# Kernel tuning notes

Hardware: AMD Instinct MI355X
Metric: run time of the kernel (lower is better)

## Reference

```python
import jax, jax.numpy as jnp
import numpy as np

B, S, D = 2, 2048, 2048
H, G = 16, 4
DH = D // H  # 128
KV = G * DH  # 512


def setup_inputs() -> dict:
    key = jax.random.key(0)
    ks = jax.random.split(key, 10)
    scale = 1.0 / np.sqrt(D)
    hidden_state = jax.random.normal(ks[0], (B, S, D), dtype=jnp.float32)
    # causal mask: 1 above the diagonal (positions to block), 0 elsewhere
    casual_mask = jnp.triu(jnp.ones((S, S), dtype=jnp.float32), k=1)
    padding_mask = jnp.zeros((B, S), dtype=jnp.float32)
    Wq = jax.random.normal(ks[1], (D, D), dtype=jnp.float32) * scale
    bq = jnp.zeros((D,), dtype=jnp.float32)
    Wk = jax.random.normal(ks[2], (D, KV), dtype=jnp.float32) * scale
    bk = jnp.zeros((KV,), dtype=jnp.float32)
    Wv = jax.random.normal(ks[3], (D, KV), dtype=jnp.float32) * scale
    bv = jnp.zeros((KV,), dtype=jnp.float32)
    Wo = jax.random.normal(ks[4], (D, D), dtype=jnp.float32) * scale
    bo = jnp.zeros((D,), dtype=jnp.float32)
    return {"hidden_state": hidden_state, "casual_mask": casual_mask,
            "padding_mask": padding_mask, "Wq": Wq, "bq": bq, "Wk": Wk,
            "bk": bk, "Wv": Wv, "bv": bv, "Wo": Wo, "bo": bo}


def reference(hidden_state, casual_mask, padding_mask, Wq, bq, Wk, bk, Wv, bv, Wo, bo):
    b, s, _ = hidden_state.shape
    rep = H // G  # heads per KV group
    q = (hidden_state @ Wq + bq).reshape(b, s, H, DH).transpose(0, 2, 1, 3)  # [b,H,s,dh]
    k = (hidden_state @ Wk + bk).reshape(b, s, G, DH).transpose(0, 2, 1, 3)  # [b,G,s,dh]
    v = (hidden_state @ Wv + bv).reshape(b, s, G, DH).transpose(0, 2, 1, 3)
    # expand KV heads: each group serves H//G query heads
    k = jnp.repeat(k, rep, axis=1)  # [b,H,s,dh]
    v = jnp.repeat(v, rep, axis=1)
    scores = jnp.einsum('bhqd,bhkd->bhqk', q, k) / jnp.sqrt(jnp.float32(DH))
    scores = scores + casual_mask * (-1e9)
    scores = scores + padding_mask[:, None, None, :] * (-1e9)
    attn = jax.nn.softmax(scores, axis=-1)
    out = jnp.einsum('bhqk,bhkd->bhqd', attn, v)  # [b,H,s,dh]
    out = out.transpose(0, 2, 1, 3).reshape(b, s, D)
    return out @ Wo + bo
```

## Files before the change

### kernel.cpp

```cpp
#include <hip/hip_runtime.h>
#include <math.h>

typedef unsigned short u16;
typedef __bf16 bf16_t;
typedef u16 u16x4 __attribute__((ext_vector_type(4)));
typedef u16 u16x8 __attribute__((ext_vector_type(8)));
typedef bf16_t bf16x8 __attribute__((ext_vector_type(8)));
typedef float f32x4 __attribute__((ext_vector_type(4)));

__device__ __forceinline__ float bf2f(u16 v) {
    union { unsigned u; float f; } x; x.u = ((unsigned)v) << 16; return x.f;
}
__device__ __forceinline__ u16 f2bf(float f) {
    union { float f; unsigned u; } x; x.f = f;
    unsigned u = x.u;
    return (u16)((u + 0x7fffu + ((u >> 16) & 1u)) >> 16);
}

__device__ __forceinline__ void gload16(const u16* g, u16* l) {
    __builtin_amdgcn_global_load_lds(
        (const __attribute__((address_space(1))) void*)g,
        (__attribute__((address_space(3))) void*)l,
        16, 0, 0);
}

#define POWS_UNITS 436

__device__ __forceinline__ bool is_bf16_input(const unsigned* __restrict__ probe) {
    unsigned w = probe[(threadIdx.x & 63) * 32771 + 7];
    unsigned b7 = (w >> 8) & 0x7f;
    bool hit = (b7 >= 0x38) && (b7 <= 0x3f);
    return __builtin_popcountll(__ballot(hit)) >= 32;
}

__global__ __launch_bounds__(256) void prep_kernel(
    const void* __restrict__ X, u16* __restrict__ Xc,
    const void* __restrict__ Wq, const void* __restrict__ Wk,
    const void* __restrict__ Wv, u16* __restrict__ WqkvT,
    const unsigned* __restrict__ probe)
{
    __shared__ u16 t[32][33];
    const bool bf = is_bf16_input(probe);
    const int bid = blockIdx.x;

    if (bid < 4096) {
        int i = (bid * 256 + threadIdx.x) * 8;
        if (bf) {
            *(u16x8*)&Xc[i] = *(const u16x8*)&((const u16*)X)[i];
        } else {
            const float* s = (const float*)X + i;
            u16x8 o;
#pragma unroll
            for (int j = 0; j < 8; j++) o[j] = f2bf(s[j]);
            *(u16x8*)&Xc[i] = o;
        }
        return;
    }

    const void* in; u16* out; int R, C, bx, by;
    if (bid < 8192) {
        int b2 = bid - 4096; in = Wq; out = WqkvT;
        R = 2048; C = 2048; bx = (b2 & 63) * 32; by = (b2 >> 6) * 32;
    } else if (bid < 9216) {
        int b2 = bid - 8192; in = Wk; out = WqkvT + 2048 * 2048;
        R = 2048; C = 512; bx = (b2 & 15) * 32; by = (b2 >> 4) * 32;
    } else {
        int b2 = bid - 9216; in = Wv; out = WqkvT + 2560 * 2048;
        R = 2048; C = 512; bx = (b2 & 15) * 32; by = (b2 >> 4) * 32;
    }
    int x = threadIdx.x & 31, y = threadIdx.x >> 5;
    if (bf) {
        const u16* s = (const u16*)in;
#pragma unroll
        for (int i = 0; i < 32; i += 8)
            t[y + i][x] = s[(size_t)(by + y + i) * C + bx + x];
    } else {
        const float* s = (const float*)in;
#pragma unroll
        for (int i = 0; i < 32; i += 8)
            t[y + i][x] = f2bf(s[(size_t)(by + y + i) * C + bx + x]);
    }
    __syncthreads();
#pragma unroll
    for (int i = 0; i < 32; i += 8)
        out[(size_t)(bx + y + i) * R + by + x] = t[x][y + i];
}

__global__ __launch_bounds__(256) void tconv_kernel(
    const void* __restrict__ in, u16* __restrict__ out, int R, int C,
    const unsigned* __restrict__ probe)
{
    bool bf = is_bf16_input(probe);
    __shared__ u16 t[32][33];
    int x = threadIdx.x & 31, y = threadIdx.x >> 5;
    int bx = blockIdx.x * 32, by = blockIdx.y * 32;
    if (bf) {
        const u16* s = (const u16*)in;
#pragma unroll
        for (int i = 0; i < 32; i += 8)
            t[y + i][x] = s[(size_t)(by + y + i) * C + bx + x];
    } else {
        const float* s = (const float*)in;
#pragma unroll
        for (int i = 0; i < 32; i += 8)
            t[y + i][x] = f2bf(s[(size_t)(by + y + i) * C + bx + x]);
    }
    __syncthreads();
#pragma unroll
    for (int i = 0; i < 32; i += 8)
        out[(size_t)(bx + y + i) * R + by + x] = t[x][y + i];
}

__global__ __launch_bounds__(256) void transpose_kernel(
    const u16* __restrict__ in, u16* __restrict__ out, int R, int LD)
{
    __shared__ u16 t[32][33];
    int x = threadIdx.x & 31, y = threadIdx.x >> 5;
    int bx = blockIdx.x * 32, by = blockIdx.y * 32;
#pragma unroll
    for (int i = 0; i < 32; i += 8)
        t[y + i][x] = in[(size_t)(by + y + i) * LD + bx + x];
    __syncthreads();
#pragma unroll
    for (int i = 0; i < 32; i += 8)
        out[(size_t)(bx + y + i) * R + by + x] = t[x][y + i];
}

__global__ __launch_bounds__(256) void gemm_bias_kernel(
    const u16* __restrict__ A, const u16* __restrict__ BT,
    const void* __restrict__ bias0, const void* __restrict__ bias1,
    const void* __restrict__ bias2, void* __restrict__ Cout,
    int M, int N, int K, const unsigned* __restrict__ probe,
    int out_native, float scale)
{
    __shared__ __align__(16) u16 As[128 * 32];
    __shared__ __align__(16) u16 Bs[128 * 32];
    const int tid  = threadIdx.x;
    const int lane = tid & 63, wave = tid >> 6;
    const int quad = lane >> 4, li = lane & 15;
    const int bm = blockIdx.x * 128, bn = blockIdx.y * 128;
    const int wm = (wave >> 1) * 64, wn = (wave & 1) * 64;
    const int lrow = lane >> 2;
    const int lcol = (lane & 3) * 8;

    f32x4 acc[4][4] = {};

    for (int k0 = 0; k0 < K; k0 += 32) {
#pragma unroll
        for (int j = 0; j < 2; j++) {
            int c = wave * 2 + j;
            int row = c * 16 + lrow;
            gload16(&A [(size_t)(bm + row) * K + k0 + lcol], &As[c * 16 * 32]);
            gload16(&BT[(size_t)(bn + row) * K + k0 + lcol], &Bs[c * 16 * 32]);
        }
        __syncthreads();
        bf16x8 af[4], bfr[4];
#pragma unroll
        for (int i = 0; i < 4; i++)
            af[i]  = *(const bf16x8*)&As[(wm + i * 16 + li) * 32 + quad * 8];
#pragma unroll
        for (int i = 0; i < 4; i++)
            bfr[i] = *(const bf16x8*)&Bs[(wn + i * 16 + li) * 32 + quad * 8];
#pragma unroll
        for (int mt = 0; mt < 4; mt++)
#pragma unroll
            for (int nt = 0; nt < 4; nt++)
                acc[mt][nt] = __builtin_amdgcn_mfma_f32_16x16x32_bf16(
                    af[mt], bfr[nt], acc[mt][nt], 0, 0, 0);
        __syncthreads();
    }

    const bool bf_in = is_bf16_input(probe);
    const bool out_bf = out_native ? bf_in : true;
#pragma unroll
    for (int nt = 0; nt < 4; nt++) {
        int col = bn + wn + nt * 16 + li;
        const void* bp; int bc;
        if (col < 2048)      { bp = bias0; bc = col; }
        else if (col < 2560) { bp = bias1; bc = col - 2048; }
        else                 { bp = bias2; bc = col - 2560; }
        float bb = bf_in ? bf2f(((const u16*)bp)[bc]) : ((const float*)bp)[bc];
        if (out_bf) {
            u16* C16 = (u16*)Cout;
#pragma unroll
            for (int mt = 0; mt < 4; mt++)
#pragma unroll
                for (int r = 0; r < 4; r++) {
                    int row = bm + wm + mt * 16 + quad * 4 + r;
                    C16[(size_t)row * N + col] = f2bf((acc[mt][nt][r] + bb) * scale);
                }
        } else {
            float* Cf = (float*)Cout;
#pragma unroll
            for (int mt = 0; mt < 4; mt++)
#pragma unroll
                for (int r = 0; r < 4; r++) {
                    int row = bm + wm + mt * 16 + quad * 4 + r;
                    Cf[(size_t)row * N + col] = (acc[mt][nt][r] + bb) * scale;
                }
        }
    }
}

__global__ __launch_bounds__(256) void flash_kernel(
    const u16* __restrict__ Q, const u16* __restrict__ Kg,
    const u16* __restrict__ VT, u16* __restrict__ O,
    float* __restrict__ POws, float* __restrict__ POdout,
    float* __restrict__ PM, float* __restrict__ PL)
{
    constexpr int S = 2048, D = 2048, DH = 128, QKSTR = 3072;
    constexpr float SCALE = 0.08838834764831845f;
    __shared__ __align__(16) u16 Ks[32 * 136];
    __shared__ __align__(16) u16 Vt[128 * 40];
    __shared__ __align__(16) u16 Pw[4][32 * 40];

    const int tid  = threadIdx.x;
    const int wave = tid >> 6, lane = tid & 63;
    const int quad = lane >> 4, li = lane & 15;
    const int uu = blockIdx.x, h = blockIdx.y, b = blockIdx.z;
    int qt, cc, nc;
    if (uu < 7)       { qt = uu;                         cc = 0;          nc = 1; }
    else if (uu < 21) { int t = uu - 7;  qt = 7 + (t >> 1);  cc = t & 1;  nc = 2; }
    else              { int t = uu - 21; qt = 14 + t / 3;    cc = t % 3;  nc = 3; }
    const int T = qt + 1;
    const int tb = T / nc, trem = T % nc;
    const int tcnt = tb + (cc < trem ? 1 : 0);
    const int tstart = cc * tb + (cc < trem ? cc : trem);
    const int kstart = tstart * 128;
    const int kend   = (tstart + tcnt) * 128;
    const int g = h >> 2;
    const int q0w = qt * 128 + wave * 32;

    const u16* Qb = Q  + (size_t)b * S * QKSTR;
    const u16* Kb = Kg + (size_t)b * S * QKSTR;
    const u16* Vg = VT + (size_t)g * DH * (2 * S) + (size_t)b * S;

    bf16x8 qf[2][4];
#pragma unroll
    for (int m = 0; m < 2; m++)
#pragma unroll
        for (int c = 0; c < 4; c++)
            qf[m][c] = *(const bf16x8*)&Qb[(size_t)(q0w + m * 16 + li) * QKSTR
                                           + h * DH + c * 32 + quad * 8];

    f32x4 oacc[2][8] = {};
    float mr[2] = { -INFINITY, -INFINITY };
    float lr[2] = { 0.f, 0.f };

    u16x8 kreg[2], vreg[2];
#pragma unroll
    for (int ch = 0; ch < 2; ch++) {
        int idx = tid + ch * 256;
        kreg[ch] = *(const u16x8*)&Kb[(size_t)(kstart + (idx >> 4)) * QKSTR
                                      + g * DH + (idx & 15) * 8];
        vreg[ch] = *(const u16x8*)&Vg[(size_t)(idx >> 2) * (2 * S)
                                      + kstart + (idx & 3) * 8];
    }

    for (int kc = kstart; kc < kend; kc += 32) {
#pragma unroll
        for (int ch = 0; ch < 2; ch++) {
            int idx = tid + ch * 256;
            *(u16x8*)&Ks[(idx >> 4) * 136 + (idx & 15) * 8] = kreg[ch];
            *(u16x8*)&Vt[(idx >> 2) * 40  + (idx & 3) * 8]  = vreg[ch];
        }
        __syncthreads();

        int kn = kc + 32;
        if (kn < kend) {
#pragma unroll
            for (int ch = 0; ch < 2; ch++) {
                int idx = tid + ch * 256;
                kreg[ch] = *(const u16x8*)&Kb[(size_t)(kn + (idx >> 4)) * QKSTR
                                              + g * DH + (idx & 15) * 8];
                vreg[ch] = *(const u16x8*)&Vg[(size_t)(idx >> 2) * (2 * S)
                                              + kn + (idx & 3) * 8];
            }
        }

        if (kc <= q0w) {
            f32x4 sacc[2][2] = {};
#pragma unroll
            for (int t = 0; t < 2; t++)
#pragma unroll
                for (int c = 0; c < 4; c++) {
                    bf16x8 kf = *(const bf16x8*)&Ks[(t * 16 + li) * 136 + c * 32 + quad * 8];
#pragma unroll
                    for (int m = 0; m < 2; m++)
                        sacc[m][t] = __builtin_amdgcn_mfma_f32_16x16x32_bf16(
                            kf, qf[m][c], sacc[m][t], 0, 0, 0);
                }

            float alpha_b[2][4];
#pragma unroll
            for (int m = 0; m < 2; m++) {
                int row = q0w + m * 16 + li;
                f32x4 s0 = sacc[m][0] * SCALE;
                f32x4 s1 = sacc[m][1] * SCALE;
#pragma unroll
                for (int r = 0; r < 4; r++) {
                    int k0 = kc + quad * 4 + r;
                    if (k0 > row)      s0[r] = -INFINITY;
                    if (k0 + 16 > row) s1[r] = -INFINITY;
                }
                float mx = fmaxf(fmaxf(fmaxf(s0[0], s0[1]), fmaxf(s0[2], s0[3])),
                                 fmaxf(fmaxf(s1[0], s1[1]), fmaxf(s1[2], s1[3])));
                mx = fmaxf(mx, __shfl_xor(mx, 16));
                mx = fmaxf(mx, __shfl_xor(mx, 32));
                float mnew = fmaxf(mr[m], mx);
                float al = __expf(mr[m] - mnew);
                mr[m] = mnew;
                f32x4 p0, p1;
                float ps = 0.f;
#pragma unroll
                for (int r = 0; r < 4; r++) {
                    p0[r] = __expf(s0[r] - mnew);
                    p1[r] = __expf(s1[r] - mnew);
                    ps += p0[r] + p1[r];
                }
                ps += __shfl_xor(ps, 16);
                ps += __shfl_xor(ps, 32);
                lr[m] = lr[m] * al + ps;
                u16x4 c0, c1;
#pragma unroll
                for (int r = 0; r < 4; r++) { c0[r] = f2bf(p0[r]); c1[r] = f2bf(p1[r]); }
                *(u16x4*)&Pw[wave][(m * 16 + li) * 40 + quad * 4]      = c0;
                *(u16x4*)&Pw[wave][(m * 16 + li) * 40 + 16 + quad * 4] = c1;
#pragma unroll
                for (int r = 0; r < 4; r++)
                    alpha_b[m][r] = __shfl(al, quad * 4 + r, 16);
            }

#pragma unroll
            for (int m = 0; m < 2; m++)
#pragma unroll
                for (int dt = 0; dt < 8; dt++)
#pragma unroll
                    for (int r = 0; r < 4; r++)
                        oacc[m][dt][r] *= alpha_b[m][r];

            asm volatile("s_waitcnt lgkmcnt(0)" ::: "memory");
            union { u16x8 u; bf16x8 bv; } pc0, pc1;
            pc0.u = *(const u16x8*)&Pw[wave][(0 * 16 + li) * 40 + quad * 8];
            pc1.u = *(const u16x8*)&Pw[wave][(1 * 16 + li) * 40 + quad * 8];
            bf16x8 pf[2] = { pc0.bv, pc1.bv };

#pragma unroll
            for (int dt = 0; dt < 8; dt++) {
                bf16x8 vf = *(const bf16x8*)&Vt[(dt * 16 + li) * 40 + quad * 8];
#pragma unroll
                for (int m = 0; m < 2; m++)
                    oacc[m][dt] = __builtin_amdgcn_mfma_f32_16x16x32_bf16(
                        pf[m], vf, oacc[m][dt], 0, 0, 0);
            }
        }
        __syncthreads();
    }

    if (nc == 1) {
        u16* Ob = O + (size_t)b * S * D;
#pragma unroll
        for (int m = 0; m < 2; m++) {
#pragma unroll
            for (int r = 0; r < 4; r++) {
                float linv = 1.0f / __shfl(lr[m], quad * 4 + r, 16);
                int row = q0w + m * 16 + quad * 4 + r;
#pragma unroll
                for (int dt = 0; dt < 8; dt++)
                    Ob[(size_t)row * D + h * DH + dt * 16 + li] =
                        f2bf(oacc[m][dt][r] * linv);
            }
        }
    } else {
        const int pl = (qt <= 13) ? (qt - 7) * 2 + cc : 14 + (qt - 14) * 3 + cc;
        const int pg = (b * 16 + h) * 20 + pl;
        float* POu = (pg < POWS_UNITS)
                   ? (POws   + (size_t)pg * 16384)
                   : (POdout + (size_t)(pg - POWS_UNITS) * 16384);
#pragma unroll
        for (int m = 0; m < 2; m++)
#pragma unroll
            for (int r = 0; r < 4; r++) {
                int rl = wave * 32 + m * 16 + quad * 4 + r;
#pragma unroll
                for (int dt = 0; dt < 8; dt++)
                    POu[rl * 128 + dt * 16 + li] = oacc[m][dt][r];
            }
        if (quad == 0) {
#pragma unroll
            for (int m = 0; m < 2; m++) {
                int rl = wave * 32 + m * 16 + li;
                PM[pg * 128 + rl] = mr[m];
                PL[pg * 128 + rl] = lr[m];
            }
        }
    }
}

__global__ __launch_bounds__(256) void combine_kernel(
    const float* __restrict__ POws, const float* __restrict__ POdout,
    const float* __restrict__ PM, const float* __restrict__ PL,
    u16* __restrict__ O)
{
    constexpr int S = 2048, D = 2048;
    const int qt = 7 + blockIdx.x, h = blockIdx.y, b = blockIdx.z;
    const int nc = (qt <= 13) ? 2 : 3;
    const int pl0 = (qt <= 13) ? (qt - 7) * 2 : 14 + (qt - 14) * 3;
    const int pg0 = (b * 16 + h) * 20 + pl0;
    const int t = threadIdx.x;
    const int row = t >> 1, half = (t & 1) * 64;

    float m[3], l[3], w[3];
    const float* p[3];
    float M = -INFINITY;
    for (int i = 0; i < nc; i++) {
        int pg = pg0 + i;
        m[i] = PM[pg * 128 + row];
        l[i] = PL[pg * 128 + row];
        M = fmaxf(M, m[i]);
        p[i] = ((pg < POWS_UNITS)
                ? (POws   + (size_t)pg * 16384)
                : (POdout + (size_t)(pg - POWS_UNITS) * 16384))
               + row * 128 + half;
    }
    float lsum = 0.f;
    for (int i = 0; i < nc; i++) { w[i] = __expf(m[i] - M); lsum += w[i] * l[i]; }
    float linv = 1.0f / lsum;

    u16* out = O + (size_t)(b * S + qt * 128 + row) * D + h * 128 + half;
#pragma unroll 4
    for (int j = 0; j < 64; j += 4) {
        f32x4 acc = {};
        for (int i = 0; i < nc; i++) {
            f32x4 a = *(const f32x4*)&p[i][j];
#pragma unroll
            for (int e = 0; e < 4; e++) acc[e] += a[e] * w[i];
        }
        u16x4 o;
#pragma unroll
        for (int e = 0; e < 4; e++) o[e] = f2bf(acc[e] * linv);
        *(u16x4*)&out[j] = o;
    }
}

extern "C" void kernel_launch(void* const* d_in, const int* in_sizes, int n_in,
                              void* d_out, int out_size, void* d_ws, size_t ws_size,
                              hipStream_t stream)
{
    const void* X  = d_in[0];
    const void* Wq = d_in[3];
    const void* bq = d_in[4];
    const void* Wk = d_in[5];
    const void* bk = d_in[6];
    const void* Wv = d_in[7];
    const void* bv = d_in[8];
    const void* Wo = d_in[9];
    const void* bo = d_in[10];
    const unsigned* probe = (const unsigned*)d_in[3];

    u16* ws    = (u16*)d_ws;
    u16* Xc    = ws;
    u16* WqkvT = Xc    + 8388608;
    u16* QKV   = WqkvT + 6291456;
    u16* VTb   = QKV   + 12582912;
    u16* Ob    = VTb   + 2097152;
    float* POws   = (float*)ws;
    float* PM     = POws + (size_t)POWS_UNITS * 16384;
    float* PL     = PM + 640 * 128;
    float* POdout = (float*)d_out;

    prep_kernel<<<10240, 256, 0, stream>>>(X, Xc, Wq, Wk, Wv, WqkvT, probe);

    gemm_bias_kernel<<<dim3(32, 24), 256, 0, stream>>>(
        Xc, WqkvT, bq, bk, bv, QKV, 4096, 3072, 2048, probe, 0, 1.0f);

    transpose_kernel<<<dim3(16, 128), 256, 0, stream>>>(QKV + 2560, VTb, 4096, 3072);

    flash_kernel<<<dim3(27, 16, 2), 256, 0, stream>>>(
        QKV, QKV + 2048, VTb, Ob, POws, POdout, PM, PL);

    combine_kernel<<<dim3(9, 16, 2), 256, 0, stream>>>(POws, POdout, PM, PL, Ob);

    tconv_kernel<<<dim3(64, 64), 256, 0, stream>>>(Wo, WqkvT, 2048, 2048, probe);

    gemm_bias_kernel<<<dim3(32, 16), 256, 0, stream>>>(
        Ob, WqkvT, bo, bo, bo, d_out, 4096, 2048, 2048, probe, 1, 1.0f);
}
```

Baseline: 416.6 us.

## Fuse V transpose into QKV GEMM epilogue and merge combine with Wo transpose

The QKV GEMM epilogue now also writes the V columns transposed into the VT buffer, so the separate transpose kernel is gone. The split-K combine and the Wo transpose/convert are merged into one launch, with the block index selecting the role. The transposed Wo is written into the QKV region, which is no longer needed at that point. This removes two kernel launches and one extra read of V, at the cost of strided scalar stores in the GEMM epilogue for V tiles.

```diff
diff --git a/kernel.cpp b/kernel.cpp
--- a/kernel.cpp
+++ b/kernel.cpp
@@ -86,52 +86,12 @@
         out[(size_t)(bx + y + i) * R + by + x] = t[x][y + i];
 }
 
-__global__ __launch_bounds__(256) void tconv_kernel(
-    const void* __restrict__ in, u16* __restrict__ out, int R, int C,
-    const unsigned* __restrict__ probe)
-{
-    bool bf = is_bf16_input(probe);
-    __shared__ u16 t[32][33];
-    int x = threadIdx.x & 31, y = threadIdx.x >> 5;
-    int bx = blockIdx.x * 32, by = blockIdx.y * 32;
-    if (bf) {
-        const u16* s = (const u16*)in;
-#pragma unroll
-        for (int i = 0; i < 32; i += 8)
-            t[y + i][x] = s[(size_t)(by + y + i) * C + bx + x];
-    } else {
-        const float* s = (const float*)in;
-#pragma unroll
-        for (int i = 0; i < 32; i += 8)
-            t[y + i][x] = f2bf(s[(size_t)(by + y + i) * C + bx + x]);
-    }
-    __syncthreads();
-#pragma unroll
-    for (int i = 0; i < 32; i += 8)
-        out[(size_t)(bx + y + i) * R + by + x] = t[x][y + i];
-}
-
-__global__ __launch_bounds__(256) void transpose_kernel(
-    const u16* __restrict__ in, u16* __restrict__ out, int R, int LD)
-{
-    __shared__ u16 t[32][33];
-    int x = threadIdx.x & 31, y = threadIdx.x >> 5;
-    int bx = blockIdx.x * 32, by = blockIdx.y * 32;
-#pragma unroll
-    for (int i = 0; i < 32; i += 8)
-        t[y + i][x] = in[(size_t)(by + y + i) * LD + bx + x];
-    __syncthreads();
-#pragma unroll
-    for (int i = 0; i < 32; i += 8)
-        out[(size_t)(bx + y + i) * R + by + x] = t[x][y + i];
-}
-
 __global__ __launch_bounds__(256) void gemm_bias_kernel(
     const u16* __restrict__ A, const u16* __restrict__ BT,
     const void* __restrict__ bias0, const void* __restrict__ bias1,
     const void* __restrict__ bias2, void* __restrict__ Cout,
     int M, int N, int K, const unsigned* __restrict__ probe,
-    int out_native, float scale)
+    int out_native, float scale, u16* __restrict__ VTdual)
 {
     __shared__ __align__(16) u16 As[128 * 32];
     __shared__ __align__(16) u16 Bs[128 * 32];
@@ -182,12 +142,16 @@
         float bb = bf_in ? bf2f(((const u16*)bp)[bc]) : ((const float*)bp)[bc];
         if (out_bf) {
             u16* C16 = (u16*)Cout;
+            const bool dv = (VTdual != nullptr) && (col >= 2560);
+            u16* vtp = dv ? &VTdual[(size_t)(col - 2560) * 4096] : nullptr;
 #pragma unroll
             for (int mt = 0; mt < 4; mt++)
 #pragma unroll
                 for (int r = 0; r < 4; r++) {
                     int row = bm + wm + mt * 16 + quad * 4 + r;
-                    C16[(size_t)row * N + col] = f2bf((acc[mt][nt][r] + bb) * scale);
+                    u16 v = f2bf((acc[mt][nt][r] + bb) * scale);
+                    C16[(size_t)row * N + col] = v;
+                    if (dv) vtp[row] = v;
                 }
         } else {
             float* Cf = (float*)Cout;
@@ -397,13 +361,42 @@
     }
 }
 
-__global__ __launch_bounds__(256) void combine_kernel(
+__global__ __launch_bounds__(256) void finish_kernel(
     const float* __restrict__ POws, const float* __restrict__ POdout,
     const float* __restrict__ PM, const float* __restrict__ PL,
-    u16* __restrict__ O)
+    u16* __restrict__ O, const void* __restrict__ Wo, u16* __restrict__ WoT,
+    const unsigned* __restrict__ probe)
 {
     constexpr int S = 2048, D = 2048;
-    const int qt = 7 + blockIdx.x, h = blockIdx.y, b = blockIdx.z;
+    __shared__ u16 ts[32][33];
+    const int bid = blockIdx.x;
+
+    if (bid < 4096) {
+        const bool bf = is_bf16_input(probe);
+        int x = threadIdx.x & 31, y = threadIdx.x >> 5;
+        int bx = (bid & 63) * 32, by = (bid >> 6) * 32;
+        if (bf) {
+            const u16* s = (const u16*)Wo;
+#pragma unroll
+            for (int i = 0; i < 32; i += 8)
+                ts[y + i][x] = s[(size_t)(by + y + i) * 2048 + bx + x];
+        } else {
+            const float* s = (const float*)Wo;
+#pragma unroll
+            for (int i = 0; i < 32; i += 8)
+                ts[y + i][x] = f2bf(s[(size_t)(by + y + i) * 2048 + bx + x]);
+        }
+        __syncthreads();
+#pragma unroll
+        for (int i = 0; i < 32; i += 8)
+            WoT[(size_t)(bx + y + i) * 2048 + by + x] = ts[x][y + i];
+        return;
+    }
+
+    const int b2 = bid - 4096;
+    const int qt = 7 + (b2 % 9);
+    const int h  = (b2 / 9) & 15;
+    const int b  = b2 / 144;
     const int nc = (qt <= 13) ? 2 : 3;
     const int pl0 = (qt <= 13) ? (qt - 7) * 2 : 14 + (qt - 14) * 3;
     const int pg0 = (b * 16 + h) * 20 + pl0;
@@ -464,6 +457,7 @@
     u16* QKV   = WqkvT + 6291456;
     u16* VTb   = QKV   + 12582912;
     u16* Ob    = VTb   + 2097152;
+    u16* WoT   = QKV;
     float* POws   = (float*)ws;
     float* PM     = POws + (size_t)POWS_UNITS * 16384;
     float* PL     = PM + 640 * 128;
@@ -472,17 +466,14 @@
     prep_kernel<<<10240, 256, 0, stream>>>(X, Xc, Wq, Wk, Wv, WqkvT, probe);
 
     gemm_bias_kernel<<<dim3(32, 24), 256, 0, stream>>>(
-        Xc, WqkvT, bq, bk, bv, QKV, 4096, 3072, 2048, probe, 0, 1.0f);
-
-    transpose_kernel<<<dim3(16, 128), 256, 0, stream>>>(QKV + 2560, VTb, 4096, 3072);
+        Xc, WqkvT, bq, bk, bv, QKV, 4096, 3072, 2048, probe, 0, 1.0f, VTb);
 
     flash_kernel<<<dim3(27, 16, 2), 256, 0, stream>>>(
         QKV, QKV + 2048, VTb, Ob, POws, POdout, PM, PL);
 
-    combine_kernel<<<dim3(9, 16, 2), 256, 0, stream>>>(POws, POdout, PM, PL, Ob);
-
-    tconv_kernel<<<dim3(64, 64), 256, 0, stream>>>(Wo, WqkvT, 2048, 2048, probe);
+    finish_kernel<<<4384, 256, 0, stream>>>(
+        POws, POdout, PM, PL, Ob, Wo, WoT, probe);
 
     gemm_bias_kernel<<<dim3(32, 16), 256, 0, stream>>>(
-        Ob, WqkvT, bo, bo, bo, d_out, 4096, 2048, 2048, probe, 1, 1.0f);
-}
+        Ob, WoT, bo, bo, bo, d_out, 4096, 2048, 2048, probe, 1, 1.0f, nullptr);
+}
```

New measurement: 435.9 us. 1.05x slower.
